# Performance work log

Hardware: AMD Instinct MI355X
Metric: run time of the kernel (lower is better)

## Reference

```python
import jax, jax.numpy as jnp
import numpy as np

B, S, H, E, V, NSTEPS = 8, 128, 512, 512, 32000, 8


def setup_inputs() -> dict:
    key = jax.random.key(0)
    ks = jax.random.split(key, 24)

    def lin(k, fi, fo):
        return (jax.random.normal(k, (fi, fo), jnp.float32) / np.sqrt(fi).astype(np.float32))

    return {
        "input_ids": jax.random.randint(ks[0], (B, S), 0, V),
        "tree_ids": jax.random.randint(ks[1], (B, NSTEPS, 3, S), 0, S),
        "emb": jax.random.normal(ks[2], (V, E), jnp.float32) * 0.02,
        "W_ioux": lin(ks[3], E, 3 * H),
        "W_iouh_r": lin(ks[4], H, 3 * H),
        "b_iouh_r": jnp.zeros((3 * H,), jnp.float32),
        "W_iouh_l": lin(ks[5], H, 3 * H),
        "b_iouh_l": jnp.zeros((3 * H,), jnp.float32),
        "W_fx": lin(ks[6], E, H),
        "W_fh0": lin(ks[7], H, H),
        "b_fh0": jnp.zeros((H,), jnp.float32),
        "W_fh1": lin(ks[8], H, H),
        "b_fh1": jnp.zeros((H,), jnp.float32),
        "W_fh2": lin(ks[9], H, H),
        "b_fh2": jnp.zeros((H,), jnp.float32),
        "W_fh3": lin(ks[10], H, H),
        "b_fh3": jnp.zeros((H,), jnp.float32),
    }


def _scatter_rows(vals, idx):
    # out[b, idx[b, j], k] += vals[b, j, k]  (torch scatter_add_ along dim 1)
    return jax.vmap(lambda v, i: jnp.zeros_like(v).at[i].add(v))(vals, idx)


def _gather_rows(vals, idx):
    # out[b, j, k] = vals[b, idx[b, j], k]  (torch gather along dim 1)
    return jnp.take_along_axis(vals, idx[:, :, None], axis=1)


def _masked_scatter(dest, mask_rows, src):
    # Exact torch masked_scatter_ semantics: flatten mask/src, fill True slots
    # with consecutive elements of flattened src.
    m = jnp.broadcast_to(mask_rows[:, :, None], dest.shape).reshape(-1)
    pos = jnp.clip(jnp.cumsum(m) - 1, 0, None)
    out = jnp.where(m, src.reshape(-1)[pos], dest.reshape(-1))
    return out.reshape(dest.shape)


def reference(input_ids, tree_ids, emb, W_ioux, W_iouh_r, b_iouh_r, W_iouh_l,
              b_iouh_l, W_fx, W_fh0, b_fh0, W_fh1, b_fh1, W_fh2, b_fh2,
              W_fh3, b_fh3):
    x = emb[input_ids]                      # [B, S, E]
    Hs = W_fx.shape[1]
    iou_x = x @ W_ioux                      # [B, S, 3H], loop-invariant
    fx_x = x @ W_fx                         # [B, S, H],  loop-invariant
    h0 = jnp.zeros(x.shape[:2] + (Hs,), x.dtype)
    c0 = jnp.zeros_like(h0)
    steps = jnp.transpose(tree_ids, (1, 0, 2, 3))  # [n_steps, B, 3, S]

    def step(carry, t):
        h, c = carry
        idx_d, idx_r, idx_l = t[:, 0], t[:, 1], t[:, 2]
        iou_hr = h @ W_iouh_r + b_iouh_r
        iou_hl = h @ W_iouh_l + b_iouh_l
        # torch scatter_add_ with an index of width H into a 3H buffer only
        # touches the first H channels -- replicate that exactly.
        scat = _scatter_rows(iou_hr[..., :Hs], idx_r) + _scatter_rows(iou_hl[..., :Hs], idx_l)
        iou = iou_x.at[..., :Hs].add(scat)
        i, o, u = jnp.split(iou, 3, axis=-1)
        i, o, u = jax.nn.sigmoid(i), jax.nn.sigmoid(o), jnp.tanh(u)
        # fh0 and fh1 share idx_r, fh2 and fh3 share idx_l -> fold linearly.
        fh_r = h @ (W_fh0 + W_fh1) + (b_fh0 + b_fh1)
        fh_l = h @ (W_fh2 + W_fh3) + (b_fh2 + b_fh3)
        f = jax.nn.sigmoid(_gather_rows(fx_x, idx_d)
                           + _gather_rows(fh_r, idx_r)
                           + _gather_rows(fh_l, idx_l))
        fc = f * c
        c_full = i * u + _scatter_rows(fc, idx_d)
        h_full = o * jnp.tanh(c_full)
        mask = idx_d != 0
        h_new = _masked_scatter(h, mask, h_full)
        c_new = _masked_scatter(c, mask, c_full)
        return (h_new, c_new), None

    (h, c), _ = jax.lax.scan(step, (h0, c0), steps)
    return h
```

## Files before the change

kernel.cpp:

```cpp
#include <hip/hip_runtime.h>
#include <hip/hip_bf16.h>

#define B_ 8
#define S_ 128
#define H_ 512
#define E_ 512
#define NST 8
#define R_ 1024
#define N2 2048
#define KD 512
#define LDA 72
#define NBLK 512
#define GRP 64

typedef __hip_bfloat16 bf16;
typedef __attribute__((ext_vector_type(8))) short v8s;
typedef __attribute__((ext_vector_type(4))) float v4f;
typedef unsigned long long u64;

__device__ __forceinline__ float sigm(float x){ return 1.0f/(1.0f + expf(-x)); }
__device__ __forceinline__ float load_in(const void* p, long long i, int isb){
    return isb ? __bfloat162float(((const bf16*)p)[i]) : ((const float*)p)[i];
}
__device__ __forceinline__ int idx_read(const int* p, int j, int is64){
    return is64 ? p[2*j] : p[j];
}
__device__ __forceinline__ unsigned short f2b(float v){
    bf16 b = __float2bfloat16(v);
    return *(unsigned short*)&b;
}

__device__ __forceinline__ float vload1f(const float* p){
    return __hip_atomic_load(p, __ATOMIC_RELAXED, __HIP_MEMORY_SCOPE_AGENT);
}
__device__ __forceinline__ void vstore1(float* p, float v){
    __hip_atomic_store(p, v, __ATOMIC_RELAXED, __HIP_MEMORY_SCOPE_AGENT);
}
__device__ __forceinline__ void vstore_hb2(unsigned short* p, unsigned short a, unsigned short b){
    unsigned int u = (unsigned)a | ((unsigned)b << 16);
    __hip_atomic_store((unsigned int*)p, u, __ATOMIC_RELAXED, __HIP_MEMORY_SCOPE_AGENT);
}
__device__ __forceinline__ v8s vload16(const unsigned short* p){
    union { u64 u[2]; v8s v; } c;
    c.u[0] = __hip_atomic_load((const u64*)p,     __ATOMIC_RELAXED, __HIP_MEMORY_SCOPE_AGENT);
    c.u[1] = __hip_atomic_load(((const u64*)p)+1, __ATOMIC_RELAXED, __HIP_MEMORY_SCOPE_AGENT);
    return c.v;
}

__device__ __forceinline__ void gsync(int* bar, int gen){
    __syncthreads();
    if (threadIdx.x == 0){
        int g = blockIdx.x >> 6;
        int* ga = bar + 64*(1+g);
        int* gd = bar + 64*(9+g);
        int old = __hip_atomic_fetch_add(ga, 1, __ATOMIC_RELAXED, __HIP_MEMORY_SCOPE_AGENT);
        if (old + 1 == GRP*gen){
            __hip_atomic_fetch_add(bar, GRP, __ATOMIC_RELAXED, __HIP_MEMORY_SCOPE_AGENT);
            while (__hip_atomic_load(bar, __ATOMIC_RELAXED, __HIP_MEMORY_SCOPE_AGENT) < NBLK*gen)
                __builtin_amdgcn_s_sleep(4);
            __hip_atomic_fetch_add(gd, 1, __ATOMIC_RELAXED, __HIP_MEMORY_SCOPE_AGENT);
        } else {
            while (__hip_atomic_load(gd, __ATOMIC_RELAXED, __HIP_MEMORY_SCOPE_AGENT) < gen)
                __builtin_amdgcn_s_sleep(4);
        }
    }
    __syncthreads();
}

__global__ void probe_all(const void* t0, const void* t1, const void* t2, const void* t3,
                          const void* t4, const void* t5, const void* t6, const void* t7,
                          const void* t8, const void* t9, const void* t10, const void* t11,
                          const void* t12, const void* t13, const void* t14,
                          const int* __restrict__ ids, const int* __restrict__ tree,
                          int* __restrict__ flags){
    const void* ts[15] = {t0,t1,t2,t3,t4,t5,t6,t7,t8,t9,t10,t11,t12,t13,t14};
    int bid = blockIdx.x, t = threadIdx.x;
    int bad = 0;
    if (bid < 15){
        if (t < 512){
            unsigned short u = ((const unsigned short*)ts[bid])[t];
            bad = (((u >> 7) & 0xFF) >= 140);
        }
    } else {
        const int* p = (bid == 15) ? ids : tree;
        int n = (bid == 15) ? 1024 : 2048;
        for (int j = t; j < n; j += 1024)
            if (j & 1) bad |= (p[j] != 0);
    }
    unsigned long long bl = __ballot(bad);
    __shared__ int acc[16];
    if ((t & 63) == 0) acc[t >> 6] = (bl != 0ull) ? 1 : 0;
    __syncthreads();
    if (t == 0){
        int any = 0;
        for (int w = 0; w < 16; ++w) any |= acc[w];
        flags[(bid < 15) ? bid : (16 + bid - 15)] = any ? 0 : 1;
    }
}

#define NB2 320
#define GS2 (NB2*512)
__global__ __launch_bounds__(512)
void rank_pack(const void* __restrict__ Wioux, const void* __restrict__ Wfx,
               const void* __restrict__ Wr, const void* __restrict__ Wl,
               const void* __restrict__ W0, const void* __restrict__ W1,
               const void* __restrict__ W2, const void* __restrict__ W3,
               const void* __restrict__ br, const void* __restrict__ bl,
               const void* __restrict__ b0, const void* __restrict__ b1,
               const void* __restrict__ b2, const void* __restrict__ b3,
               const int* __restrict__ ids, const void* __restrict__ emb,
               const int* __restrict__ tree,
               unsigned short* __restrict__ WxT, unsigned short* __restrict__ WcatT,
               float* __restrict__ bcat, unsigned short* __restrict__ xb,
               float* __restrict__ h0,
               int* __restrict__ msk, int* __restrict__ rnk, int* __restrict__ cnt,
               const int* __restrict__ flags, int* __restrict__ bar){
    int bid = blockIdx.x, tid = threadIdx.x;
    int is64 = flags[17];
    if (bid == 0){
        for (int i = tid; i < 64*17; i += 512) bar[i] = 0;
    }
    if (bid < 8){
        int st = bid;
        for (int c = tid; c < R_; c += 512){
            cnt[(0*NST + st)*R_ + c] = 0;
            cnt[(1*NST + st)*R_ + c] = 0;
            cnt[(2*NST + st)*R_ + c] = 0;
        }
        __syncthreads();
        __shared__ int wt[8];
        int runbase = 0;
        for (int ch = 0; ch < 2; ++ch){
            int t = ch*512 + tid;
            int b = t >> 7, s = t & 127;
            int base = (b*NST + st)*3*S_;
            int d0 = idx_read(tree, base + s, is64);
            int rd = (b<<7) + d0;
            int rr = (b<<7) + idx_read(tree, base + S_ + s, is64);
            int rl = (b<<7) + idx_read(tree, base + 2*S_ + s, is64);
            int m = (d0 != 0) ? 1 : 0;
            unsigned long long bal = __ballot(m);
            int lane = tid & 63, wv = tid >> 6;
            if (lane == 0) wt[wv] = __popcll(bal);
            __syncthreads();
            int bp = runbase, tot = 0;
            for (int w = 0; w < wv; ++w) bp += wt[w];
            for (int w = 0; w < 8; ++w) tot += wt[w];
            int rank = bp + __popcll(bal & ((1ull << lane) - 1ull));
            msk[st*R_ + t] = m;
            rnk[st*R_ + t] = m ? rank : 0;
            atomicAdd(&cnt[(0*NST + st)*R_ + rr], 1);
            atomicAdd(&cnt[(1*NST + st)*R_ + rl], 1);
            atomicAdd(&cnt[(2*NST + st)*R_ + rd], 1);
            runbase += tot;
            __syncthreads();
        }
    }
    int gt = bid*512 + tid;
    {
        int f_wx = flags[1], f_wf = flags[6];
        for (int u = gt; u < 131072; u += GS2){
            int n = u >> 6, k0 = (u & 63)*8;
            unsigned short tmp[8];
            #pragma unroll
            for (int i = 0; i < 8; ++i){
                float v = (n < 1536) ? load_in(Wioux, (long long)(k0+i)*1536 + n, f_wx)
                                     : load_in(Wfx,   (long long)(k0+i)*512 + (n-1536), f_wf);
                tmp[i] = f2b(v);
            }
            *(v8s*)&WxT[(size_t)n*KD + k0] = *(v8s*)tmp;
        }
    }
    {
        int fWr=flags[2], fWl=flags[4], fW0=flags[7], fW1=flags[9], fW2=flags[11], fW3=flags[13];
        for (int u = gt; u < 131072; u += GS2){
            int n = u >> 6, k0 = (u & 63)*8;
            unsigned short tmp[8];
            #pragma unroll
            for (int i = 0; i < 8; ++i){
                long long k = k0 + i;
                float v;
                if      (n <  512) v = load_in(Wr, k*1536 + n, fWr);
                else if (n < 1024) v = load_in(Wl, k*1536 + (n-512), fWl);
                else if (n < 1536) { int c = n-1024; v = load_in(W0, k*512+c, fW0) + load_in(W1, k*512+c, fW1); }
                else               { int c = n-1536; v = load_in(W2, k*512+c, fW2) + load_in(W3, k*512+c, fW3); }
                tmp[i] = f2b(v);
            }
            *(v8s*)&WcatT[(size_t)n*KD + k0] = *(v8s*)tmp;
        }
    }
    {
        int fbr=flags[3], fbl=flags[5], fb0=flags[8], fb1=flags[10], fb2=flags[12], fb3=flags[14];
        for (int n = gt; n < 2048; n += GS2){
            float v;
            if      (n <  512) v = load_in(br, n, fbr);
            else if (n < 1024) v = load_in(bl, n-512, fbl);
            else if (n < 1536) v = load_in(b0, n-1024, fb0) + load_in(b1, n-1024, fb1);
            else               v = load_in(b2, n-1536, fb2) + load_in(b3, n-1536, fb3);
            bcat[n] = v;
        }
    }
    {
        int f_emb = flags[0], i64i = flags[16];
        for (int u = gt; u < 65536; u += GS2){
            int r = u >> 6, c0 = (u & 63)*8;
            long long base = (long long)idx_read(ids, r, i64i)*E_ + c0;
            unsigned short tmp[8];
            #pragma unroll
            for (int i = 0; i < 8; ++i) tmp[i] = f2b(load_in(emb, base + i, f_emb));
            *(v8s*)&xb[(size_t)r*KD + c0] = *(v8s*)tmp;
        }
    }
    for (int u = gt; u < 262144; u += GS2)
        ((float4*)h0)[u] = make_float4(0.f,0.f,0.f,0.f);
}

__global__ void csr_scan(const int* __restrict__ cnt, int* __restrict__ off,
                         int* __restrict__ cur){
    int st = blockIdx.x, a = blockIdx.y;
    int t = threadIdx.x;
    int base = (a*NST + st)*R_;
    __shared__ int sh[R_];
    int v = cnt[base + t];
    sh[t] = v;
    __syncthreads();
    for (int d = 1; d < R_; d <<= 1){
        int x = (t >= d) ? sh[t - d] : 0;
        __syncthreads();
        sh[t] += x;
        __syncthreads();
    }
    int excl = sh[t] - v;
    off[base + t] = excl;
    cur[base + t] = excl;
}

__global__ __launch_bounds__(512)
void csr_fill(const int* __restrict__ tree, int* __restrict__ cur,
              int* __restrict__ ent, const int* __restrict__ flags){
    int is64 = flags[17];
    int st = blockIdx.x;
    for (int ch = 0; ch < 2; ++ch){
        int t = ch*512 + threadIdx.x;
        int b = t >> 7, s = t & 127;
        int base = (b*NST + st)*3*S_;
        int rd = (b<<7) + idx_read(tree, base + s, is64);
        int rr = (b<<7) + idx_read(tree, base + S_ + s, is64);
        int rl = (b<<7) + idx_read(tree, base + 2*S_ + s, is64);
        int p0 = atomicAdd(&cur[(0*NST + st)*R_ + rr], 1);
        ent[(0*NST + st)*R_ + p0] = t;
        int p1 = atomicAdd(&cur[(1*NST + st)*R_ + rl], 1);
        ent[(1*NST + st)*R_ + p1] = t;
        int p2 = atomicAdd(&cur[(2*NST + st)*R_ + rd], 1);
        ent[(2*NST + st)*R_ + p2] = t | (rr << 10) | (rl << 20);
    }
}

__device__ __forceinline__ void gemm_phase(const unsigned short* __restrict__ A,
               const unsigned short* __restrict__ BT,
               const float* __restrict__ bias,
               float* __restrict__ C,
               short* __restrict__ SMEM)
{
    int bid = blockIdx.x;
    int bn = (bid & 7)*4 + ((bid >> 3) & 3);
    int bm = bid >> 5;
    int tid = threadIdx.x;
    int lane = tid & 63, wave = tid >> 6;
    int grp = wave >> 2, w4 = wave & 3;
    int wm = w4 & 1, wn = w4 >> 1;
    int lm = lane & 15, quad = lane >> 4;
    short* As = SMEM + grp*(2*64*LDA);
    short* Bs = As + 64*LDA;
    v4f acc[2][2];
    #pragma unroll
    for (int i=0;i<2;++i)
        #pragma unroll
        for (int j=0;j<2;++j) acc[i][j] = (v4f)0.0f;

    int t = tid & 255;
    int srow = t >> 3, sg = (t & 7)*8;
    int kb = grp*256;
    const unsigned short* Ab = A  + (size_t)(bm*64)*KD + kb;
    const unsigned short* Bb = BT + (size_t)(bn*64)*KD + kb;
    v8s pa[2], pb[2];
    #pragma unroll
    for (int j=0;j<2;++j){
        pa[j] = vload16(Ab + (size_t)(j*32+srow)*KD + sg);
        pb[j] = *(const v8s*)(Bb + (size_t)(j*32+srow)*KD + sg);
    }
    for (int k0 = 0; k0 < 256; k0 += 64){
        #pragma unroll
        for (int j=0;j<2;++j){
            *(v8s*)&As[(j*32+srow)*LDA + sg] = pa[j];
            *(v8s*)&Bs[(j*32+srow)*LDA + sg] = pb[j];
        }
        __syncthreads();
        int k1 = k0 + 64;
        if (k1 < 256){
            #pragma unroll
            for (int j=0;j<2;++j){
                pa[j] = vload16(Ab + (size_t)(j*32+srow)*KD + k1 + sg);
                pb[j] = *(const v8s*)(Bb + (size_t)(j*32+srow)*KD + k1 + sg);
            }
        }
        #pragma unroll
        for (int kk = 0; kk < 64; kk += 32){
            v8s af[2], bf[2];
            #pragma unroll
            for (int i=0;i<2;++i){
                af[i] = *(const v8s*)&As[(wm*32 + i*16 + lm)*LDA + kk + quad*8];
                bf[i] = *(const v8s*)&Bs[(wn*32 + i*16 + lm)*LDA + kk + quad*8];
            }
            #pragma unroll
            for (int i=0;i<2;++i)
                #pragma unroll
                for (int j=0;j<2;++j)
                    acc[i][j] = __builtin_amdgcn_mfma_f32_16x16x32_bf16(af[i], bf[j], acc[i][j], 0, 0, 0);
        }
        __syncthreads();
    }
    float* Red = (float*)SMEM;
    if (grp){
        #pragma unroll
        for (int i=0;i<2;++i)
            #pragma unroll
            for (int j=0;j<2;++j)
                #pragma unroll
                for (int rg=0;rg<4;++rg)
                    Red[(wm*32 + i*16 + quad*4 + rg)*64 + (wn*32 + j*16 + lm)] = acc[i][j][rg];
    }
    __syncthreads();
    if (!grp){
        #pragma unroll
        for (int j=0;j<2;++j){
            int n = bn*64 + wn*32 + j*16 + lm;
            float bv = bias ? bias[n] : 0.0f;
            #pragma unroll
            for (int i=0;i<2;++i){
                int m0 = bm*64 + wm*32 + i*16 + quad*4;
                #pragma unroll
                for (int rg = 0; rg < 4; ++rg){
                    float v = acc[i][j][rg] + Red[(wm*32 + i*16 + quad*4 + rg)*64 + (wn*32 + j*16 + lm)] + bv;
                    vstore1(&C[(size_t)(m0+rg)*N2 + n], v);
                }
            }
        }
    }
}

__device__ __forceinline__ void epi_phase(const float* __restrict__ XO,
              const float* __restrict__ T, int tstr,
              const float* __restrict__ hc, const float* __restrict__ cc,
              float* __restrict__ hn, float* __restrict__ cn,
              unsigned short* __restrict__ hb, float* __restrict__ out,
              const int* __restrict__ msk, const int* __restrict__ rnk,
              const int* __restrict__ cnt, const int* __restrict__ off,
              const int* __restrict__ ent, int st, int last)
{
    int c = threadIdx.x;
    #pragma unroll
    for (int rr2 = 0; rr2 < 2; ++rr2){
        int r = blockIdx.x*2 + rr2;
        if (!msk[st*R_ + r]){
            float hv = vload1f(&hc[(size_t)r*H_ + c]);
            if (last){
                out[(size_t)r*H_ + c] = hv;
            } else {
                vstore1(&hn[(size_t)r*H_ + c], hv);
                vstore1(&cn[(size_t)r*H_ + c], vload1f(&cc[(size_t)r*H_ + c]));
                unsigned v16 = f2b(hv);
                unsigned o16 = __shfl_down((int)v16, 1);
                if (!(c & 1)) vstore_hb2(&hb[(size_t)r*KD + c], (unsigned short)v16, (unsigned short)o16);
            }
            continue;
        }
        int j = rnk[st*R_ + r];
        int bR = off[(0*NST+st)*R_ + j], dR = cnt[(0*NST+st)*R_ + j];
        int bL = off[(1*NST+st)*R_ + j], dL = cnt[(1*NST+st)*R_ + j];
        int bD = off[(2*NST+st)*R_ + j], dD = cnt[(2*NST+st)*R_ + j];
        const int* eR = ent + (0*NST+st)*R_ + bR;
        const int* eL = ent + (1*NST+st)*R_ + bL;
        const int* eD = ent + (2*NST+st)*R_ + bD;
        const float* xo = XO + (size_t)j*N2;
        float scv = 0.f;
        {
            int e = 0;
            for (; e + 4 <= dR; e += 4){
                int a0=eR[e], a1=eR[e+1], a2=eR[e+2], a3=eR[e+3];
                float t0 = vload1f(&T[(size_t)a0*tstr + c]);
                float t1 = vload1f(&T[(size_t)a1*tstr + c]);
                float t2 = vload1f(&T[(size_t)a2*tstr + c]);
                float t3 = vload1f(&T[(size_t)a3*tstr + c]);
                scv += (t0 + t1) + (t2 + t3);
            }
            for (; e < dR; ++e) scv += vload1f(&T[(size_t)eR[e]*tstr + c]);
        }
        {
            int e = 0;
            for (; e + 4 <= dL; e += 4){
                int a0=eL[e], a1=eL[e+1], a2=eL[e+2], a3=eL[e+3];
                float t0 = vload1f(&T[(size_t)a0*tstr + 512 + c]);
                float t1 = vload1f(&T[(size_t)a1*tstr + 512 + c]);
                float t2 = vload1f(&T[(size_t)a2*tstr + 512 + c]);
                float t3 = vload1f(&T[(size_t)a3*tstr + 512 + c]);
                scv += (t0 + t1) + (t2 + t3);
            }
            for (; e < dL; ++e) scv += vload1f(&T[(size_t)eL[e]*tstr + 512 + c]);
        }
        float fxv = vload1f(&xo[1536 + c]);
        float csc = 0.f;
        {
            int e = 0;
            for (; e + 2 <= dD; e += 2){
                int p0 = eD[e], p1 = eD[e+1];
                int s0 = p0 & 1023, ra0 = (p0 >> 10) & 1023, rb0 = (p0 >> 20) & 1023;
                int s1 = p1 & 1023, ra1 = (p1 >> 10) & 1023, rb1 = (p1 >> 20) & 1023;
                float ta0 = vload1f(&T[(size_t)ra0*tstr + 1024 + c]);
                float tb0 = vload1f(&T[(size_t)rb0*tstr + 1536 + c]);
                float cv0 = vload1f(&cc[(size_t)s0*H_ + c]);
                float ta1 = vload1f(&T[(size_t)ra1*tstr + 1024 + c]);
                float tb1 = vload1f(&T[(size_t)rb1*tstr + 1536 + c]);
                float cv1 = vload1f(&cc[(size_t)s1*H_ + c]);
                csc += sigm(fxv + ta0 + tb0) * cv0 + sigm(fxv + ta1 + tb1) * cv1;
            }
            for (; e < dD; ++e){
                int pk = eD[e];
                int s  = pk & 1023, ra = (pk >> 10) & 1023, rb = (pk >> 20) & 1023;
                float ta = vload1f(&T[(size_t)ra*tstr + 1024 + c]);
                float tb = vload1f(&T[(size_t)rb*tstr + 1536 + c]);
                float cv = vload1f(&cc[(size_t)s*H_ + c]);
                csc += sigm(fxv + ta + tb) * cv;
            }
        }
        float ig = sigm(vload1f(&xo[c]) + scv);
        float og = sigm(vload1f(&xo[512 + c]));
        float ug = tanhf(vload1f(&xo[1024 + c]));
        float cf = ig*ug + csc;
        float hf = og * tanhf(cf);
        if (last){
            out[(size_t)r*H_ + c] = hf;
        } else {
            vstore1(&hn[(size_t)r*H_ + c], hf);
            vstore1(&cn[(size_t)r*H_ + c], cf);
            unsigned v16 = f2b(hf);
            unsigned o16 = __shfl_down((int)v16, 1);
            if (!(c & 1)) vstore_hb2(&hb[(size_t)r*KD + c], (unsigned short)v16, (unsigned short)o16);
        }
    }
}

__global__ __launch_bounds__(512, 4)
void chain_all(const unsigned short* __restrict__ xb,
               const unsigned short* __restrict__ WxT,
               const unsigned short* __restrict__ WcatT,
               const float* __restrict__ bcat,
               float* __restrict__ XO, float* __restrict__ T,
               float* __restrict__ h0, float* __restrict__ c0,
               float* __restrict__ h1, float* __restrict__ c1,
               unsigned short* __restrict__ hb, float* __restrict__ out,
               const int* __restrict__ msk, const int* __restrict__ rnk,
               const int* __restrict__ cnt, const int* __restrict__ off,
               const int* __restrict__ ent, int* bar)
{
    __shared__ short SMEM[4*64*LDA];
    int gen = 0;

    gemm_phase(xb, WxT, (const float*)nullptr, XO, SMEM);
    gsync(bar, ++gen);
    epi_phase(XO, bcat, 0, h0, c0, h1, c1, hb, out, msk, rnk, cnt, off, ent, 0, 0);
    gsync(bar, ++gen);

    for (int st = 1; st < NST; ++st){
        const float* hcp = (st & 1) ? h1 : h0;
        const float* ccp = (st & 1) ? c1 : c0;
        float* hnp = (st & 1) ? h0 : h1;
        float* cnp = (st & 1) ? c0 : c1;
        gemm_phase(hb, WcatT, bcat, T, SMEM);
        gsync(bar, ++gen);
        epi_phase(XO, T, N2, hcp, ccp, hnp, cnp, hb, out,
                  msk, rnk, cnt, off, ent, st, (st == NST-1) ? 1 : 0);
        if (st < NST-1) gsync(bar, ++gen);
    }
}

extern "C" void kernel_launch(void* const* d_in, const int* in_sizes, int n_in,
                              void* d_out, int out_size, void* d_ws, size_t ws_size,
                              hipStream_t stream) {
    const int* input_ids = (const int*)d_in[0];
    const int* tree      = (const int*)d_in[1];

    char* wp = (char*)d_ws;
    auto alloc = [&](size_t bytes) -> void* {
        void* q = (void*)wp;
        wp += (bytes + 255) & ~(size_t)255;
        return q;
    };
    float*          XO     = (float*)alloc((size_t)R_*N2*4);
    float*          T      = (float*)alloc((size_t)R_*N2*4);
    float*          h0     = (float*)alloc((size_t)R_*H_*4);
    float*          c0     = (float*)alloc((size_t)R_*H_*4);
    float*          h1     = (float*)alloc((size_t)R_*H_*4);
    float*          c1     = (float*)alloc((size_t)R_*H_*4);
    unsigned short* WxT    = (unsigned short*)alloc((size_t)N2*KD*2);
    unsigned short* WcatT  = (unsigned short*)alloc((size_t)N2*KD*2);
    float*          bcat   = (float*)alloc((size_t)N2*4);
    unsigned short* xb     = (unsigned short*)alloc((size_t)R_*KD*2);
    unsigned short* hb     = (unsigned short*)alloc((size_t)R_*KD*2);
    int*            msk    = (int*)alloc((size_t)NST*R_*4);
    int*            rnk    = (int*)alloc((size_t)NST*R_*4);
    int*            cnt    = (int*)alloc((size_t)3*NST*R_*4);
    int*            off    = (int*)alloc((size_t)3*NST*R_*4);
    int*            cur    = (int*)alloc((size_t)3*NST*R_*4);
    int*            ent    = (int*)alloc((size_t)3*NST*R_*4);
    int*            flags  = (int*)alloc(256);
    int*            bar    = (int*)alloc(8192);
    float*          out    = (float*)d_out;

    hipLaunchKernelGGL(probe_all, dim3(17), dim3(1024), 0, stream,
                       d_in[2], d_in[3], d_in[4], d_in[5], d_in[6], d_in[7], d_in[8],
                       d_in[9], d_in[10], d_in[11], d_in[12], d_in[13], d_in[14],
                       d_in[15], d_in[16], input_ids, tree, flags);
    hipLaunchKernelGGL(rank_pack, dim3(NB2), dim3(512), 0, stream,
                       d_in[3], d_in[8],
                       d_in[4], d_in[6], d_in[9], d_in[11], d_in[13], d_in[15],
                       d_in[5], d_in[7], d_in[10], d_in[12], d_in[14], d_in[16],
                       input_ids, d_in[2], tree,
                       WxT, WcatT, bcat, xb, h0, msk, rnk, cnt, flags, bar);
    hipLaunchKernelGGL(csr_scan, dim3(NST, 3), dim3(1024), 0, stream, cnt, off, cur);
    hipLaunchKernelGGL(csr_fill, dim3(NST), dim3(512), 0, stream, tree, cur, ent, flags);

    hipLaunchKernelGGL(chain_all, dim3(NBLK), dim3(512), 0, stream,
                       xb, WxT, WcatT, bcat, XO, T, h0, c0, h1, c1, hb, out,
                       msk, rnk, cnt, off, ent, bar);
}
```

Baseline: 295.5 us.

## Interleave XO columns for vector loads, prefetch A tiles, unroll gathers, widen csr_fill

The x-projection GEMM now stores XO with the four gate columns interleaved, so the epilogue reads i/o/u/f with a single 16-byte load instead of four scalar loads. The GEMM prefetches all four A k-tiles into registers up front rather than double-buffering them. The gather loops are unrolled further (8-way for scatter sums, 4-way for the forget-gate sum) to expose more independent loads. The barrier sleep is shortened and csr_fill is split over more, smaller blocks. In exchange, register pressure rises (pa grows to eight vectors), which could affect occupancy under launch_bounds(512,4).

```diff
diff --git a/kernel.cpp b/kernel.cpp
--- a/kernel.cpp
+++ b/kernel.cpp
@@ -33,6 +33,12 @@
 __device__ __forceinline__ float vload1f(const float* p){
     return __hip_atomic_load(p, __ATOMIC_RELAXED, __HIP_MEMORY_SCOPE_AGENT);
 }
+__device__ __forceinline__ float4 vload4f(const float* p){
+    union { u64 u[2]; float4 f; } c;
+    c.u[0] = __hip_atomic_load((const u64*)p,     __ATOMIC_RELAXED, __HIP_MEMORY_SCOPE_AGENT);
+    c.u[1] = __hip_atomic_load(((const u64*)p)+1, __ATOMIC_RELAXED, __HIP_MEMORY_SCOPE_AGENT);
+    return c.f;
+}
 __device__ __forceinline__ void vstore1(float* p, float v){
     __hip_atomic_store(p, v, __ATOMIC_RELAXED, __HIP_MEMORY_SCOPE_AGENT);
 }
@@ -57,11 +63,11 @@
         if (old + 1 == GRP*gen){
             __hip_atomic_fetch_add(bar, GRP, __ATOMIC_RELAXED, __HIP_MEMORY_SCOPE_AGENT);
             while (__hip_atomic_load(bar, __ATOMIC_RELAXED, __HIP_MEMORY_SCOPE_AGENT) < NBLK*gen)
-                __builtin_amdgcn_s_sleep(4);
+                __builtin_amdgcn_s_sleep(2);
             __hip_atomic_fetch_add(gd, 1, __ATOMIC_RELAXED, __HIP_MEMORY_SCOPE_AGENT);
         } else {
             while (__hip_atomic_load(gd, __ATOMIC_RELAXED, __HIP_MEMORY_SCOPE_AGENT) < gen)
-                __builtin_amdgcn_s_sleep(4);
+                __builtin_amdgcn_s_sleep(2);
         }
     }
     __syncthreads();
@@ -235,31 +241,29 @@
     cur[base + t] = excl;
 }
 
-__global__ __launch_bounds__(512)
+__global__ __launch_bounds__(128)
 void csr_fill(const int* __restrict__ tree, int* __restrict__ cur,
               int* __restrict__ ent, const int* __restrict__ flags){
     int is64 = flags[17];
-    int st = blockIdx.x;
-    for (int ch = 0; ch < 2; ++ch){
-        int t = ch*512 + threadIdx.x;
-        int b = t >> 7, s = t & 127;
-        int base = (b*NST + st)*3*S_;
-        int rd = (b<<7) + idx_read(tree, base + s, is64);
-        int rr = (b<<7) + idx_read(tree, base + S_ + s, is64);
-        int rl = (b<<7) + idx_read(tree, base + 2*S_ + s, is64);
-        int p0 = atomicAdd(&cur[(0*NST + st)*R_ + rr], 1);
-        ent[(0*NST + st)*R_ + p0] = t;
-        int p1 = atomicAdd(&cur[(1*NST + st)*R_ + rl], 1);
-        ent[(1*NST + st)*R_ + p1] = t;
-        int p2 = atomicAdd(&cur[(2*NST + st)*R_ + rd], 1);
-        ent[(2*NST + st)*R_ + p2] = t | (rr << 10) | (rl << 20);
-    }
+    int st = blockIdx.x >> 3;
+    int t  = ((blockIdx.x & 7) << 7) + threadIdx.x;
+    int b = t >> 7, s = t & 127;
+    int base = (b*NST + st)*3*S_;
+    int rd = (b<<7) + idx_read(tree, base + s, is64);
+    int rr = (b<<7) + idx_read(tree, base + S_ + s, is64);
+    int rl = (b<<7) + idx_read(tree, base + 2*S_ + s, is64);
+    int p0 = atomicAdd(&cur[(0*NST + st)*R_ + rr], 1);
+    ent[(0*NST + st)*R_ + p0] = t;
+    int p1 = atomicAdd(&cur[(1*NST + st)*R_ + rl], 1);
+    ent[(1*NST + st)*R_ + p1] = t;
+    int p2 = atomicAdd(&cur[(2*NST + st)*R_ + rd], 1);
+    ent[(2*NST + st)*R_ + p2] = t | (rr << 10) | (rl << 20);
 }
 
 __device__ __forceinline__ void gemm_phase(const unsigned short* __restrict__ A,
                const unsigned short* __restrict__ BT,
                const float* __restrict__ bias,
-               float* __restrict__ C,
+               float* __restrict__ C, int pack,
                short* __restrict__ SMEM)
 {
     int bid = blockIdx.x;
@@ -283,26 +287,27 @@
     int kb = grp*256;
     const unsigned short* Ab = A  + (size_t)(bm*64)*KD + kb;
     const unsigned short* Bb = BT + (size_t)(bn*64)*KD + kb;
-    v8s pa[2], pb[2];
+    v8s pa[4][2], pb[2];
     #pragma unroll
-    for (int j=0;j<2;++j){
-        pa[j] = vload16(Ab + (size_t)(j*32+srow)*KD + sg);
+    for (int q=0;q<4;++q)
+        #pragma unroll
+        for (int j=0;j<2;++j)
+            pa[q][j] = vload16(Ab + (size_t)(j*32+srow)*KD + q*64 + sg);
+    #pragma unroll
+    for (int j=0;j<2;++j)
         pb[j] = *(const v8s*)(Bb + (size_t)(j*32+srow)*KD + sg);
-    }
-    for (int k0 = 0; k0 < 256; k0 += 64){
+    #pragma unroll
+    for (int q = 0; q < 4; ++q){
         #pragma unroll
         for (int j=0;j<2;++j){
-            *(v8s*)&As[(j*32+srow)*LDA + sg] = pa[j];
+            *(v8s*)&As[(j*32+srow)*LDA + sg] = pa[q][j];
             *(v8s*)&Bs[(j*32+srow)*LDA + sg] = pb[j];
         }
         __syncthreads();
-        int k1 = k0 + 64;
-        if (k1 < 256){
-            #pragma unroll
-            for (int j=0;j<2;++j){
-                pa[j] = vload16(Ab + (size_t)(j*32+srow)*KD + k1 + sg);
-                pb[j] = *(const v8s*)(Bb + (size_t)(j*32+srow)*KD + k1 + sg);
-            }
+        if (q < 3){
+            #pragma unroll
+            for (int j=0;j<2;++j)
+                pb[j] = *(const v8s*)(Bb + (size_t)(j*32+srow)*KD + (q+1)*64 + sg);
         }
         #pragma unroll
         for (int kk = 0; kk < 64; kk += 32){
@@ -336,13 +341,14 @@
         for (int j=0;j<2;++j){
             int n = bn*64 + wn*32 + j*16 + lm;
             float bv = bias ? bias[n] : 0.0f;
+            int noff = pack ? (((n & 511) << 2) + (n >> 9)) : n;
             #pragma unroll
             for (int i=0;i<2;++i){
                 int m0 = bm*64 + wm*32 + i*16 + quad*4;
                 #pragma unroll
                 for (int rg = 0; rg < 4; ++rg){
                     float v = acc[i][j][rg] + Red[(wm*32 + i*16 + quad*4 + rg)*64 + (wn*32 + j*16 + lm)] + bv;
-                    vstore1(&C[(size_t)(m0+rg)*N2 + n], v);
+                    vstore1(&C[(size_t)(m0+rg)*N2 + noff], v);
                 }
             }
         }
@@ -356,12 +362,12 @@
               unsigned short* __restrict__ hb, float* __restrict__ out,
               const int* __restrict__ msk, const int* __restrict__ rnk,
               const int* __restrict__ cnt, const int* __restrict__ off,
-              const int* __restrict__ ent, int st, int last)
+              const int* __restrict__ ent, int st, int last, int r0)
 {
     int c = threadIdx.x;
     #pragma unroll
     for (int rr2 = 0; rr2 < 2; ++rr2){
-        int r = blockIdx.x*2 + rr2;
+        int r = r0 + rr2;
         if (!msk[st*R_ + r]){
             float hv = vload1f(&hc[(size_t)r*H_ + c]);
             if (last){
@@ -382,47 +388,76 @@
         const int* eR = ent + (0*NST+st)*R_ + bR;
         const int* eL = ent + (1*NST+st)*R_ + bL;
         const int* eD = ent + (2*NST+st)*R_ + bD;
-        const float* xo = XO + (size_t)j*N2;
+        float4 x4 = vload4f(XO + (size_t)j*N2 + (size_t)c*4);
         float scv = 0.f;
         {
             int e = 0;
+            for (; e + 8 <= dR; e += 8){
+                float t0 = vload1f(&T[(size_t)eR[e  ]*tstr + c]);
+                float t1 = vload1f(&T[(size_t)eR[e+1]*tstr + c]);
+                float t2 = vload1f(&T[(size_t)eR[e+2]*tstr + c]);
+                float t3 = vload1f(&T[(size_t)eR[e+3]*tstr + c]);
+                float t4 = vload1f(&T[(size_t)eR[e+4]*tstr + c]);
+                float t5 = vload1f(&T[(size_t)eR[e+5]*tstr + c]);
+                float t6 = vload1f(&T[(size_t)eR[e+6]*tstr + c]);
+                float t7 = vload1f(&T[(size_t)eR[e+7]*tstr + c]);
+                scv += ((t0 + t1) + (t2 + t3)) + ((t4 + t5) + (t6 + t7));
+            }
             for (; e + 4 <= dR; e += 4){
-                int a0=eR[e], a1=eR[e+1], a2=eR[e+2], a3=eR[e+3];
-                float t0 = vload1f(&T[(size_t)a0*tstr + c]);
-                float t1 = vload1f(&T[(size_t)a1*tstr + c]);
-                float t2 = vload1f(&T[(size_t)a2*tstr + c]);
-                float t3 = vload1f(&T[(size_t)a3*tstr + c]);
+                float t0 = vload1f(&T[(size_t)eR[e  ]*tstr + c]);
+                float t1 = vload1f(&T[(size_t)eR[e+1]*tstr + c]);
+                float t2 = vload1f(&T[(size_t)eR[e+2]*tstr + c]);
+                float t3 = vload1f(&T[(size_t)eR[e+3]*tstr + c]);
                 scv += (t0 + t1) + (t2 + t3);
             }
             for (; e < dR; ++e) scv += vload1f(&T[(size_t)eR[e]*tstr + c]);
         }
         {
             int e = 0;
+            for (; e + 8 <= dL; e += 8){
+                float t0 = vload1f(&T[(size_t)eL[e  ]*tstr + 512 + c]);
+                float t1 = vload1f(&T[(size_t)eL[e+1]*tstr + 512 + c]);
+                float t2 = vload1f(&T[(size_t)eL[e+2]*tstr + 512 + c]);
+                float t3 = vload1f(&T[(size_t)eL[e+3]*tstr + 512 + c]);
+                float t4 = vload1f(&T[(size_t)eL[e+4]*tstr + 512 + c]);
+                float t5 = vload1f(&T[(size_t)eL[e+5]*tstr + 512 + c]);
+                float t6 = vload1f(&T[(size_t)eL[e+6]*tstr + 512 + c]);
+                float t7 = vload1f(&T[(size_t)eL[e+7]*tstr + 512 + c]);
+                scv += ((t0 + t1) + (t2 + t3)) + ((t4 + t5) + (t6 + t7));
+            }
             for (; e + 4 <= dL; e += 4){
-                int a0=eL[e], a1=eL[e+1], a2=eL[e+2], a3=eL[e+3];
-                float t0 = vload1f(&T[(size_t)a0*tstr + 512 + c]);
-                float t1 = vload1f(&T[(size_t)a1*tstr + 512 + c]);
-                float t2 = vload1f(&T[(size_t)a2*tstr + 512 + c]);
-                float t3 = vload1f(&T[(size_t)a3*tstr + 512 + c]);
+                float t0 = vload1f(&T[(size_t)eL[e  ]*tstr + 512 + c]);
+                float t1 = vload1f(&T[(size_t)eL[e+1]*tstr + 512 + c]);
+                float t2 = vload1f(&T[(size_t)eL[e+2]*tstr + 512 + c]);
+                float t3 = vload1f(&T[(size_t)eL[e+3]*tstr + 512 + c]);
                 scv += (t0 + t1) + (t2 + t3);
             }
             for (; e < dL; ++e) scv += vload1f(&T[(size_t)eL[e]*tstr + 512 + c]);
         }
-        float fxv = vload1f(&xo[1536 + c]);
+        float fxv = x4.w;
         float csc = 0.f;
         {
             int e = 0;
-            for (; e + 2 <= dD; e += 2){
-                int p0 = eD[e], p1 = eD[e+1];
+            for (; e + 4 <= dD; e += 4){
+                int p0 = eD[e], p1 = eD[e+1], p2 = eD[e+2], p3 = eD[e+3];
                 int s0 = p0 & 1023, ra0 = (p0 >> 10) & 1023, rb0 = (p0 >> 20) & 1023;
                 int s1 = p1 & 1023, ra1 = (p1 >> 10) & 1023, rb1 = (p1 >> 20) & 1023;
+                int s2 = p2 & 1023, ra2 = (p2 >> 10) & 1023, rb2 = (p2 >> 20) & 1023;
+                int s3 = p3 & 1023, ra3 = (p3 >> 10) & 1023, rb3 = (p3 >> 20) & 1023;
                 float ta0 = vload1f(&T[(size_t)ra0*tstr + 1024 + c]);
                 float tb0 = vload1f(&T[(size_t)rb0*tstr + 1536 + c]);
                 float cv0 = vload1f(&cc[(size_t)s0*H_ + c]);
                 float ta1 = vload1f(&T[(size_t)ra1*tstr + 1024 + c]);
                 float tb1 = vload1f(&T[(size_t)rb1*tstr + 1536 + c]);
                 float cv1 = vload1f(&cc[(size_t)s1*H_ + c]);
-                csc += sigm(fxv + ta0 + tb0) * cv0 + sigm(fxv + ta1 + tb1) * cv1;
+                float ta2 = vload1f(&T[(size_t)ra2*tstr + 1024 + c]);
+                float tb2 = vload1f(&T[(size_t)rb2*tstr + 1536 + c]);
+                float cv2 = vload1f(&cc[(size_t)s2*H_ + c]);
+                float ta3 = vload1f(&T[(size_t)ra3*tstr + 1024 + c]);
+                float tb3 = vload1f(&T[(size_t)rb3*tstr + 1536 + c]);
+                float cv3 = vload1f(&cc[(size_t)s3*H_ + c]);
+                csc += (sigm(fxv + ta0 + tb0) * cv0 + sigm(fxv + ta1 + tb1) * cv1)
+                     + (sigm(fxv + ta2 + tb2) * cv2 + sigm(fxv + ta3 + tb3) * cv3);
             }
             for (; e < dD; ++e){
                 int pk = eD[e];
@@ -433,9 +468,9 @@
                 csc += sigm(fxv + ta + tb) * cv;
             }
         }
-        float ig = sigm(vload1f(&xo[c]) + scv);
-        float og = sigm(vload1f(&xo[512 + c]));
-        float ug = tanhf(vload1f(&xo[1024 + c]));
+        float ig = sigm(x4.x + scv);
+        float og = sigm(x4.y);
+        float ug = tanhf(x4.z);
         float cf = ig*ug + csc;
         float hf = og * tanhf(cf);
         if (last){
@@ -464,11 +499,12 @@
                const int* __restrict__ ent, int* bar)
 {
     __shared__ short SMEM[4*64*LDA];
+    int r0 = blockIdx.x*2;
     int gen = 0;
 
-    gemm_phase(xb, WxT, (const float*)nullptr, XO, SMEM);
+    gemm_phase(xb, WxT, (const float*)nullptr, XO, 1, SMEM);
     gsync(bar, ++gen);
-    epi_phase(XO, bcat, 0, h0, c0, h1, c1, hb, out, msk, rnk, cnt, off, ent, 0, 0);
+    epi_phase(XO, bcat, 0, h0, c0, h1, c1, hb, out, msk, rnk, cnt, off, ent, 0, 0, r0);
     gsync(bar, ++gen);
 
     for (int st = 1; st < NST; ++st){
@@ -476,10 +512,10 @@
         const float* ccp = (st & 1) ? c1 : c0;
         float* hnp = (st & 1) ? h0 : h1;
         float* cnp = (st & 1) ? c0 : c1;
-        gemm_phase(hb, WcatT, bcat, T, SMEM);
+        gemm_phase(hb, WcatT, bcat, T, 0, SMEM);
         gsync(bar, ++gen);
         epi_phase(XO, T, N2, hcp, ccp, hnp, cnp, hb, out,
-                  msk, rnk, cnt, off, ent, st, (st == NST-1) ? 1 : 0);
+                  msk, rnk, cnt, off, ent, st, (st == NST-1) ? 1 : 0, r0);
         if (st < NST-1) gsync(bar, ++gen);
     }
 }
@@ -528,7 +564,7 @@
                        input_ids, d_in[2], tree,
                        WxT, WcatT, bcat, xb, h0, msk, rnk, cnt, flags, bar);
     hipLaunchKernelGGL(csr_scan, dim3(NST, 3), dim3(1024), 0, stream, cnt, off, cur);
-    hipLaunchKernelGGL(csr_fill, dim3(NST), dim3(512), 0, stream, tree, cur, ent, flags);
+    hipLaunchKernelGGL(csr_fill, dim3(NST*8), dim3(128), 0, stream, tree, cur, ent, flags);
 
     hipLaunchKernelGGL(chain_all, dim3(NBLK), dim3(512), 0, stream,
                        xb, WxT, WcatT, bcat, XO, T, h0, c0, h1, c1, hb, out,
```

After: 319.6 us. +8.1%, slower.
